# Performance work log

Hardware: AMD Instinct MI355X
Metric: run time of the kernel (lower is better)

## Reference

```python
import jax, jax.numpy as jnp
import numpy as np


def setup_inputs() -> dict:
    key = jax.random.key(0)
    k1, k2 = jax.random.split(key)
    B, C, H, W = 32, 8, 256, 256
    inp = jax.random.normal(k1, (B, C, H, W), dtype=jnp.float32)
    tgt = jax.random.uniform(k2, (B, C, H, W), dtype=jnp.float32)
    return {"input": inp, "target": tgt}


def reference(input, target):
    B, C, H, W = input.shape
    # DSNT: softmax over each flattened heatmap -> expected (x, y) coords
    probs = jax.nn.softmax(input.reshape(B, C, H * W), axis=-1).reshape(B, C, H, W)
    xs = (jnp.arange(1, W + 1, dtype=input.dtype) / W)  # (j+1)/x_size
    ys = (jnp.arange(1, H + 1, dtype=input.dtype) / H)  # (p+1)/y_size
    pred_x = jnp.einsum('bchw,w->bc', probs, xs)
    pred_y = jnp.einsum('bchw,h->bc', probs, ys)
    # ground truth: argmax of target heatmap -> grid coords
    am = jnp.argmax(target.reshape(B, C, H * W), axis=-1)  # [B,C] int
    true_x = ((am % W) + 1).astype(input.dtype) / W
    true_y = ((am // W) + 1).astype(input.dtype) / H
    ed = jnp.sqrt((true_x - pred_x) ** 2 + (true_y - pred_y) ** 2)  # [B,C]
    # original sums over all (b,c) and divides by (i+1) == batch size B
    return (jnp.sum(ed) / B).reshape(1)
```

## Files before the change

kernel.cpp:

```cpp
#include <hip/hip_runtime.h>
#include <float.h>
#include <math.h>


#define HW 65536
#define SPLITS 4
#define K1_BLOCK 512
#define CHUNK (HW / SPLITS)
#define NF4 (CHUNK / 4 / K1_BLOCK)

__global__ __launch_bounds__(K1_BLOCK) void dsnt_partial_kernel(
    const float* __restrict__ inp,
    const float* __restrict__ tgt,
    float* __restrict__ ws,
    int np)
{
    const int blk = blockIdx.x;
    const int bc  = blk >> 2;
    const int s   = blk & 3;
    const int t   = threadIdx.x;

    const float4* in4 = (const float4*)(inp + (size_t)bc * HW) + s * (CHUNK / 4);
    const float4* tg4 = (const float4*)(tgt + (size_t)bc * HW) + s * (CHUNK / 4);
    const int ebase = s * CHUNK;

    const float inv256 = 1.0f / 256.0f;

    float4 xa[NF4], ga[NF4];
#pragma unroll
    for (int k = 0; k < NF4; ++k) xa[k] = in4[t + k * K1_BLOCK];
#pragma unroll
    for (int k = 0; k < NF4; ++k) ga[k] = tg4[t + k * K1_BLOCK];

    float l = 0.0f, sx = 0.0f, sy = 0.0f;
#pragma unroll
    for (int k = 0; k < NF4; ++k) {
        const float4 x = xa[k];
        const int e0 = ebase + (t + k * K1_BLOCK) * 4;
        const float ex = __expf(x.x);
        const float ey = __expf(x.y);
        const float ez = __expf(x.z);
        const float ew = __expf(x.w);
        const float es = (ex + ey) + (ez + ew);

        const int   w0 = e0 & 255;
        const int   hh = e0 >> 8;
        l  += es;
        sy += (float)(hh + 1) * inv256 * es;
        sx += (ex * (float)(w0 + 1) + ey * (float)(w0 + 2)
             + ez * (float)(w0 + 3) + ew * (float)(w0 + 4)) * inv256;
    }

    float bv = -FLT_MAX;
    int   bi = 0;
#pragma unroll
    for (int k = 0; k < NF4; ++k) {
        const float4 g = ga[k];
        const int e0 = ebase + (t + k * K1_BLOCK) * 4;
        if (g.x > bv) { bv = g.x; bi = e0;     }
        if (g.y > bv) { bv = g.y; bi = e0 + 1; }
        if (g.z > bv) { bv = g.z; bi = e0 + 2; }
        if (g.w > bv) { bv = g.w; bi = e0 + 3; }
    }

#pragma unroll
    for (int off = 32; off > 0; off >>= 1) {
        l  += __shfl_down(l,  off);
        sx += __shfl_down(sx, off);
        sy += __shfl_down(sy, off);
        const float bv2 = __shfl_down(bv, off);
        const int   bi2 = __shfl_down(bi, off);
        if (bv2 > bv || (bv2 == bv && bi2 < bi)) { bv = bv2; bi = bi2; }
    }

    __shared__ float sl[8], ssx[8], ssy[8], sbv[8];
    __shared__ int   sbi[8];
    const int wid  = t >> 6;
    const int lane = t & 63;
    if (lane == 0) {
        sl[wid] = l; ssx[wid] = sx; ssy[wid] = sy;
        sbv[wid] = bv; sbi[wid] = bi;
    }
    __syncthreads();

    if (t == 0) {
        l = sl[0]; sx = ssx[0]; sy = ssy[0]; bv = sbv[0]; bi = sbi[0];
#pragma unroll
        for (int i = 1; i < 8; ++i) {
            l += sl[i]; sx += ssx[i]; sy += ssy[i];
            if (sbv[i] > bv || (sbv[i] == bv && sbi[i] < bi)) { bv = sbv[i]; bi = sbi[i]; }
        }
        ws[blk]          = l;
        ws[np + blk]     = sx;
        ws[2 * np + blk] = sy;
        ws[3 * np + blk] = bv;
        ((int*)ws)[4 * np + blk] = bi;
    }
}

__global__ __launch_bounds__(256) void dsnt_final_kernel(
    const float* __restrict__ ws,
    float* __restrict__ out,
    int nbc, int np)
{
    const int i = threadIdx.x;
    const float inv256 = 1.0f / 256.0f;
    float ed = 0.0f;

    if (i < nbc) {
        const int j0 = i * SPLITS;
        float l  = ws[j0];
        float sx = ws[np + j0];
        float sy = ws[2 * np + j0];
        float bv = ws[3 * np + j0];
        int   bi = ((const int*)ws)[4 * np + j0];
#pragma unroll
        for (int j = 1; j < SPLITS; ++j) {
            const int jj = j0 + j;
            l  += ws[jj];
            sx += ws[np + jj];
            sy += ws[2 * np + jj];
            const float bvj = ws[3 * np + jj];
            const int   bij = ((const int*)ws)[4 * np + jj];
            if (bvj > bv || (bvj == bv && bij < bi)) { bv = bvj; bi = bij; }
        }
        const float px = sx / l;
        const float py = sy / l;
        const float tx = (float)((bi & 255) + 1) * inv256;
        const float ty = (float)((bi >> 8) + 1) * inv256;
        const float dx = tx - px;
        const float dy = ty - py;
        ed = sqrtf(dx * dx + dy * dy);
    }

#pragma unroll
    for (int off = 32; off > 0; off >>= 1)
        ed += __shfl_down(ed, off);

    __shared__ float sw[4];
    if ((i & 63) == 0) sw[i >> 6] = ed;
    __syncthreads();
    if (i == 0)
        out[0] = (sw[0] + sw[1] + sw[2] + sw[3]) * (1.0f / 32.0f);
}

extern "C" void kernel_launch(void* const* d_in, const int* in_sizes, int n_in,
                              void* d_out, int out_size, void* d_ws, size_t ws_size,
                              hipStream_t stream) {
    const float* inp = (const float*)d_in[0];
    const float* tgt = (const float*)d_in[1];
    float* out = (float*)d_out;
    float* ws  = (float*)d_ws;

    const int nbc = in_sizes[0] / HW;
    const int np  = nbc * SPLITS;

    dsnt_partial_kernel<<<np, K1_BLOCK, 0, stream>>>(inp, tgt, ws, np);
    dsnt_final_kernel<<<1, 256, 0, stream>>>(ws, out, nbc, np);
}
```

Baseline: 143.8 us.

## Stage inputs through LDS with direct global-to-LDS loads and smaller blocks

Replaces per-thread register loads with __builtin_amdgcn_global_load_lds copies of each 4096-float chunk of input and target into shared memory, then reads them back as float4. It also splits each heatmap into 16 blocks of 256 threads instead of 4 blocks of 512, and merges the softmax and argmax loops. The goal is to issue memory traffic asynchronously, lower register pressure and raise occupancy on this bandwidth-bound reduction. The cost is 32KB of LDS per block, an extra LDS round trip, and four times as many partial results for the final kernel to combine.

```diff
diff --git a/kernel.cpp b/kernel.cpp
--- a/kernel.cpp
+++ b/kernel.cpp
@@ -1,42 +1,69 @@
 #include <hip/hip_runtime.h>
 #include <float.h>
 #include <math.h>
+#include <stdint.h>
 
 
 #define HW 65536
-#define SPLITS 4
-#define K1_BLOCK 512
-#define CHUNK (HW / SPLITS)
-#define NF4 (CHUNK / 4 / K1_BLOCK)
+#define BLOCK 256
+#define CHUNK_F 4096
+#define NB (HW / CHUNK_F)
+#define NF4 (CHUNK_F / 4 / BLOCK)
 
-__global__ __launch_bounds__(K1_BLOCK) void dsnt_partial_kernel(
+typedef const __attribute__((address_space(1))) unsigned int* gbl_u32;
+typedef __attribute__((address_space(3))) unsigned int* lds_u32;
+
+__device__ __forceinline__ void gl2lds16(const float* g, float* l) {
+    __builtin_amdgcn_global_load_lds((gbl_u32)g, (lds_u32)l, 16, 0, 0);
+}
+
+__global__ __launch_bounds__(BLOCK) void dsnt_partial_kernel(
     const float* __restrict__ inp,
     const float* __restrict__ tgt,
     float* __restrict__ ws,
     int np)
 {
-    const int blk = blockIdx.x;
-    const int bc  = blk >> 2;
-    const int s   = blk & 3;
-    const int t   = threadIdx.x;
+    __shared__ float s_in[CHUNK_F];
+    __shared__ float s_tg[CHUNK_F];
 
-    const float4* in4 = (const float4*)(inp + (size_t)bc * HW) + s * (CHUNK / 4);
-    const float4* tg4 = (const float4*)(tgt + (size_t)bc * HW) + s * (CHUNK / 4);
-    const int ebase = s * CHUNK;
+    const int blk  = blockIdx.x;
+    const int bc   = blk >> 4;
+    const int s    = blk & 15;
+    const int t    = threadIdx.x;
+    const int wid  = t >> 6;
+    const int lane = t & 63;
+
+    const float* gin = inp + (size_t)bc * HW + s * CHUNK_F;
+    const float* gtg = tgt + (size_t)bc * HW + s * CHUNK_F;
+    const int ebase = s * CHUNK_F;
+
+    {
+        const float* gi = gin + wid * 1024 + lane * 4;
+        const float* gt = gtg + wid * 1024 + lane * 4;
+        float* si = s_in + wid * 1024;
+        float* st = s_tg + wid * 1024;
+#pragma unroll
+        for (int j = 0; j < 4; ++j) {
+            gl2lds16(gi + j * 256, si + j * 256);
+            gl2lds16(gt + j * 256, st + j * 256);
+        }
+    }
+    __syncthreads();
 
     const float inv256 = 1.0f / 256.0f;
-
-    float4 xa[NF4], ga[NF4];
-#pragma unroll
-    for (int k = 0; k < NF4; ++k) xa[k] = in4[t + k * K1_BLOCK];
-#pragma unroll
-    for (int k = 0; k < NF4; ++k) ga[k] = tg4[t + k * K1_BLOCK];
+    const float4* si4 = (const float4*)s_in;
+    const float4* st4 = (const float4*)s_tg;
 
     float l = 0.0f, sx = 0.0f, sy = 0.0f;
+    float bv = -FLT_MAX;
+    int   bi = 0;
 #pragma unroll
     for (int k = 0; k < NF4; ++k) {
-        const float4 x = xa[k];
-        const int e0 = ebase + (t + k * K1_BLOCK) * 4;
+        const int f4 = t + k * BLOCK;
+        const float4 x = si4[f4];
+        const float4 g = st4[f4];
+        const int e0 = ebase + f4 * 4;
+
         const float ex = __expf(x.x);
         const float ey = __expf(x.y);
         const float ez = __expf(x.z);
@@ -49,14 +76,7 @@
         sy += (float)(hh + 1) * inv256 * es;
         sx += (ex * (float)(w0 + 1) + ey * (float)(w0 + 2)
              + ez * (float)(w0 + 3) + ew * (float)(w0 + 4)) * inv256;
-    }
 
-    float bv = -FLT_MAX;
-    int   bi = 0;
-#pragma unroll
-    for (int k = 0; k < NF4; ++k) {
-        const float4 g = ga[k];
-        const int e0 = ebase + (t + k * K1_BLOCK) * 4;
         if (g.x > bv) { bv = g.x; bi = e0;     }
         if (g.y > bv) { bv = g.y; bi = e0 + 1; }
         if (g.z > bv) { bv = g.z; bi = e0 + 2; }
@@ -73,10 +93,8 @@
         if (bv2 > bv || (bv2 == bv && bi2 < bi)) { bv = bv2; bi = bi2; }
     }
 
-    __shared__ float sl[8], ssx[8], ssy[8], sbv[8];
-    __shared__ int   sbi[8];
-    const int wid  = t >> 6;
-    const int lane = t & 63;
+    __shared__ float sl[4], ssx[4], ssy[4], sbv[4];
+    __shared__ int   sbi[4];
     if (lane == 0) {
         sl[wid] = l; ssx[wid] = sx; ssy[wid] = sy;
         sbv[wid] = bv; sbi[wid] = bi;
@@ -86,7 +104,7 @@
     if (t == 0) {
         l = sl[0]; sx = ssx[0]; sy = ssy[0]; bv = sbv[0]; bi = sbi[0];
 #pragma unroll
-        for (int i = 1; i < 8; ++i) {
+        for (int i = 1; i < 4; ++i) {
             l += sl[i]; sx += ssx[i]; sy += ssy[i];
             if (sbv[i] > bv || (sbv[i] == bv && sbi[i] < bi)) { bv = sbv[i]; bi = sbi[i]; }
         }
@@ -108,14 +126,14 @@
     float ed = 0.0f;
 
     if (i < nbc) {
-        const int j0 = i * SPLITS;
+        const int j0 = i * NB;
         float l  = ws[j0];
         float sx = ws[np + j0];
         float sy = ws[2 * np + j0];
         float bv = ws[3 * np + j0];
         int   bi = ((const int*)ws)[4 * np + j0];
 #pragma unroll
-        for (int j = 1; j < SPLITS; ++j) {
+        for (int j = 1; j < NB; ++j) {
             const int jj = j0 + j;
             l  += ws[jj];
             sx += ws[np + jj];
@@ -153,8 +171,8 @@
     float* ws  = (float*)d_ws;
 
     const int nbc = in_sizes[0] / HW;
-    const int np  = nbc * SPLITS;
+    const int np  = nbc * NB;
 
-    dsnt_partial_kernel<<<np, K1_BLOCK, 0, stream>>>(inp, tgt, ws, np);
+    dsnt_partial_kernel<<<np, BLOCK, 0, stream>>>(inp, tgt, ws, np);
     dsnt_final_kernel<<<1, 256, 0, stream>>>(ws, out, nbc, np);
 }
```

Measured after the change: 151.9 us. 1.06x slower.
